# Optimization experiments

Hardware: AMD Instinct MI355X
Metric: run time of the kernel (lower is better)

Reference implementation:

```python
import jax, jax.numpy as jnp
import numpy as np

B, L = 4096, 4096

# 16 power-series exponents applied to each of the 4 physical params
PS_POWERS = jnp.array([-5.0, -4.0, -3.0, -2.0, -1.5, -1.0, -0.5, 0.0,
                       0.5, 2.0, 1.0/3.0, 3.0, 0.25, 4.0, 0.2, 5.0], dtype=jnp.float32)
# polynomial exponents of the ansatz y(eta)
POLY_POWERS = jnp.array([2.0, 5.0, 8.0, 11.0, 14.0], dtype=jnp.float32)


def setup_inputs() -> dict:
    key = jax.random.key(0)
    k1, k2, k3, k4, k5, k6 = jax.random.split(key, 6)
    # positive inputs: negative/fractional powers require x > 0
    physical_params = jax.random.uniform(k1, (B, 4), jnp.float32, minval=0.1, maxval=2.0)
    eta = jax.random.uniform(k2, (B, L), jnp.float32, minval=0.1, maxval=2.0)
    # MLP params: Linear(64, 32) and Linear(32, 5), torch layout [out, in]
    W1 = jax.random.normal(k3, (32, 64), jnp.float32) * (1.0 / np.sqrt(64.0))
    b1 = jax.random.normal(k4, (32,), jnp.float32) * 0.05
    W2 = jax.random.normal(k5, (5, 32), jnp.float32) * (1.0 / np.sqrt(32.0))
    b2 = jax.random.normal(k6, (5,), jnp.float32) * 0.05
    return {"physical_params": physical_params, "eta": eta,
            "W1": W1, "b1": b1, "W2": W2, "b2": b2}


def reference(physical_params, eta, W1, b1, W2, b2):
    # power-series transform: [B,4] -> [B,4,16] -> [B,64]
    t = (physical_params[:, :, None] ** PS_POWERS).reshape(physical_params.shape[0], -1)
    # global (scalar) normalization; torch .std() is unbiased (ddof=1)
    mean = t.mean()
    std = jnp.std(t, ddof=1)
    norm = (t - mean) / std
    # network = Sequential(ReLU, Linear(64,32), Linear(32,5)) -- ReLU first, no act between linears
    h = jnp.maximum(norm, 0.0) @ W1.T + b1            # [B, 32]
    coefficients = h @ W2.T + b2                       # [B, 5]
    # dy/deta[i,j] = sum_k c[i,k] * p_k * eta[i,j]^(p_k - 1)  (vectorizes the per-row loop)
    eta_pows = eta[:, :, None] ** (POLY_POWERS - 1.0)  # [B, L, 5]
    dy_deta = jnp.einsum('bk,bjk->bj', coefficients * POLY_POWERS, eta_pows)  # [B, L]
    return dy_deta
```

## Files before the change

### kernel.cpp

```cpp
#include <hip/hip_runtime.h>
#include <math.h>

static constexpr int B  = 4096;
static constexpr int L  = 4096;
static constexpr int NT = B * 64;
static constexpr int RED_BLOCKS  = 256;
static constexpr int RED_THREADS = 256;

__device__ __constant__ float c_ps_powers[16] = {
    -5.0f, -4.0f, -3.0f, -2.0f, -1.5f, -1.0f, -0.5f, 0.0f,
     0.5f,  2.0f,  0.33333334f, 3.0f, 0.25f, 4.0f, 0.2f, 5.0f};

__device__ __constant__ float c_poly[5] = {2.0f, 5.0f, 8.0f, 11.0f, 14.0f};

__global__ __launch_bounds__(RED_THREADS)
void k_reduce_partial(const float* __restrict__ pp, double* __restrict__ part) {
    const int tid = threadIdx.x;
    const int gid = blockIdx.x * RED_THREADS + tid;
    double s = 0.0, s2 = 0.0;
    for (int i = gid; i < NT; i += RED_BLOCKS * RED_THREADS) {
        const int b = i >> 6;
        const int j = i & 63;
        const float x = pp[(b << 2) + (j >> 4)];
        const float t = powf(x, c_ps_powers[j & 15]);
        s  += (double)t;
        s2 += (double)t * (double)t;
    }
    __shared__ double sh_s[RED_THREADS];
    __shared__ double sh_s2[RED_THREADS];
    sh_s[tid] = s; sh_s2[tid] = s2;
    __syncthreads();
    for (int off = RED_THREADS >> 1; off > 0; off >>= 1) {
        if (tid < off) {
            sh_s[tid]  += sh_s[tid + off];
            sh_s2[tid] += sh_s2[tid + off];
        }
        __syncthreads();
    }
    if (tid == 0) {
        part[blockIdx.x]              = sh_s[0];
        part[RED_BLOCKS + blockIdx.x] = sh_s2[0];
    }
}

__global__ __launch_bounds__(RED_BLOCKS)
void k_finalize(const double* __restrict__ part, float* __restrict__ stats) {
    const int tid = threadIdx.x;
    __shared__ double sh_s[RED_BLOCKS];
    __shared__ double sh_s2[RED_BLOCKS];
    sh_s[tid]  = part[tid];
    sh_s2[tid] = part[RED_BLOCKS + tid];
    __syncthreads();
    for (int off = RED_BLOCKS >> 1; off > 0; off >>= 1) {
        if (tid < off) {
            sh_s[tid]  += sh_s[tid + off];
            sh_s2[tid] += sh_s2[tid + off];
        }
        __syncthreads();
    }
    if (tid == 0) {
        const double n    = (double)NT;
        const double mean = sh_s[0] / n;
        const double var  = (sh_s2[0] - n * mean * mean) / (n - 1.0);
        stats[0] = (float)mean;
        stats[1] = (float)(1.0 / sqrt(var));
    }
}

__device__ __forceinline__ float poly_eval(float e, float c0, float c1,
                                           float c2, float c3, float c4) {
    const float e3 = e * e * e;
    float w   = e;
    float acc = c0 * w;
    w *= e3;
    acc = fmaf(c1, w, acc);
    w *= e3;
    acc = fmaf(c2, w, acc);
    w *= e3;
    acc = fmaf(c3, w, acc);
    w *= e3;
    acc = fmaf(c4, w, acc);
    return acc;
}

__global__ __launch_bounds__(256)
void k_main(const float* __restrict__ pp,  const float* __restrict__ eta,
            const float* __restrict__ W1,  const float* __restrict__ b1,
            const float* __restrict__ W2,  const float* __restrict__ b2,
            const float* __restrict__ stats, float* __restrict__ out) {
    const int row = blockIdx.x;
    const int tid = threadIdx.x;

    __shared__ float sh_r[64];
    __shared__ float sh_h[32];
    __shared__ float sh_c[5];

    const float mean    = stats[0];
    const float inv_std = stats[1];

    if (tid < 64) {
        const float x = pp[(row << 2) + (tid >> 4)];
        const float t = powf(x, c_ps_powers[tid & 15]);
        sh_r[tid] = fmaxf((t - mean) * inv_std, 0.0f);
    }
    __syncthreads();

    if (tid < 32) {
        float acc = b1[tid];
        const float* w = W1 + tid * 64;
        #pragma unroll
        for (int j = 0; j < 64; ++j) acc = fmaf(sh_r[j], w[j], acc);
        sh_h[tid] = acc;
    }
    __syncthreads();

    if (tid < 5) {
        float acc = b2[tid];
        const float* w = W2 + tid * 32;
        #pragma unroll
        for (int o = 0; o < 32; ++o) acc = fmaf(sh_h[o], w[o], acc);
        sh_c[tid] = acc * c_poly[tid];
    }
    __syncthreads();

    const float c0 = sh_c[0], c1 = sh_c[1], c2 = sh_c[2],
                c3 = sh_c[3], c4 = sh_c[4];

    const float4* ep = reinterpret_cast<const float4*>(eta + (size_t)row * L);
    float4*       op = reinterpret_cast<float4*>(out + (size_t)row * L);

    #pragma unroll
    for (int i = tid; i < L / 4; i += 256) {
        const float4 e = ep[i];
        float4 r;
        r.x = poly_eval(e.x, c0, c1, c2, c3, c4);
        r.y = poly_eval(e.y, c0, c1, c2, c3, c4);
        r.z = poly_eval(e.z, c0, c1, c2, c3, c4);
        r.w = poly_eval(e.w, c0, c1, c2, c3, c4);
        op[i] = r;
    }
}

extern "C" void kernel_launch(void* const* d_in, const int* in_sizes, int n_in,
                              void* d_out, int out_size, void* d_ws, size_t ws_size,
                              hipStream_t stream) {
    const float* pp  = (const float*)d_in[0];
    const float* eta = (const float*)d_in[1];
    const float* W1  = (const float*)d_in[2];
    const float* b1  = (const float*)d_in[3];
    const float* W2  = (const float*)d_in[4];
    const float* b2  = (const float*)d_in[5];
    float* out = (float*)d_out;

    double* part = (double*)d_ws;
    float*  stats = (float*)(part + 2 * RED_BLOCKS);

    k_reduce_partial<<<RED_BLOCKS, RED_THREADS, 0, stream>>>(pp, part);
    k_finalize<<<1, RED_BLOCKS, 0, stream>>>(part, stats);
    k_main<<<B, 256, 0, stream>>>(pp, eta, W1, b1, W2, b2, stats, out);
}
```

Before: 37.07 us.

## Merge stats reduction into one kernel, use hardware log2/exp2, nontemporal IO

Replaces the two-kernel partial/finalize reduction with one single-block kernel in which each thread loads each param once, takes log2 once and evaluates all 16 powers with hardware exp2. This removes one kernel launch and the repeated powf calls. The main kernel also uses hardware log2/exp2 for the power series and nontemporal loads/stores for the eta/out stream. Hardware approximations lower precision compared with powf, and a single block leaves most of the GPU idle during the stats phase.

```diff
diff --git a/kernel.cpp b/kernel.cpp
--- a/kernel.cpp
+++ b/kernel.cpp
@@ -3,9 +3,10 @@
 
 static constexpr int B  = 4096;
 static constexpr int L  = 4096;
-static constexpr int NT = B * 64;
-static constexpr int RED_BLOCKS  = 256;
-static constexpr int RED_THREADS = 256;
+static constexpr int NX = B * 4;
+static constexpr int STATS_THREADS = 1024;
+
+typedef float f4 __attribute__((ext_vector_type(4)));
 
 __device__ __constant__ float c_ps_powers[16] = {
     -5.0f, -4.0f, -3.0f, -2.0f, -1.5f, -1.0f, -0.5f, 0.0f,
@@ -13,24 +14,32 @@
 
 __device__ __constant__ float c_poly[5] = {2.0f, 5.0f, 8.0f, 11.0f, 14.0f};
 
-__global__ __launch_bounds__(RED_THREADS)
-void k_reduce_partial(const float* __restrict__ pp, double* __restrict__ part) {
+__device__ __forceinline__ float hw_log2(float x) { return __builtin_amdgcn_logf(x); }
+__device__ __forceinline__ float hw_exp2(float x) { return __builtin_amdgcn_exp2f(x); }
+
+__global__ __launch_bounds__(STATS_THREADS)
+void k_stats(const float* __restrict__ pp, float* __restrict__ stats) {
     const int tid = threadIdx.x;
-    const int gid = blockIdx.x * RED_THREADS + tid;
     double s = 0.0, s2 = 0.0;
-    for (int i = gid; i < NT; i += RED_BLOCKS * RED_THREADS) {
-        const int b = i >> 6;
-        const int j = i & 63;
-        const float x = pp[(b << 2) + (j >> 4)];
-        const float t = powf(x, c_ps_powers[j & 15]);
-        s  += (double)t;
-        s2 += (double)t * (double)t;
+    #pragma unroll
+    for (int k = 0; k < NX / STATS_THREADS; ++k) {
+        const float x  = pp[tid + k * STATS_THREADS];
+        const float lx = hw_log2(x);
+        float sf = 0.0f, sf2 = 0.0f;
+        #pragma unroll
+        for (int p = 0; p < 16; ++p) {
+            const float t = hw_exp2(c_ps_powers[p] * lx);
+            sf  += t;
+            sf2 = fmaf(t, t, sf2);
+        }
+        s  += (double)sf;
+        s2 += (double)sf2;
     }
-    __shared__ double sh_s[RED_THREADS];
-    __shared__ double sh_s2[RED_THREADS];
+    __shared__ double sh_s[STATS_THREADS];
+    __shared__ double sh_s2[STATS_THREADS];
     sh_s[tid] = s; sh_s2[tid] = s2;
     __syncthreads();
-    for (int off = RED_THREADS >> 1; off > 0; off >>= 1) {
+    for (int off = STATS_THREADS >> 1; off > 0; off >>= 1) {
         if (tid < off) {
             sh_s[tid]  += sh_s[tid + off];
             sh_s2[tid] += sh_s2[tid + off];
@@ -38,28 +47,7 @@
         __syncthreads();
     }
     if (tid == 0) {
-        part[blockIdx.x]              = sh_s[0];
-        part[RED_BLOCKS + blockIdx.x] = sh_s2[0];
-    }
-}
-
-__global__ __launch_bounds__(RED_BLOCKS)
-void k_finalize(const double* __restrict__ part, float* __restrict__ stats) {
-    const int tid = threadIdx.x;
-    __shared__ double sh_s[RED_BLOCKS];
-    __shared__ double sh_s2[RED_BLOCKS];
-    sh_s[tid]  = part[tid];
-    sh_s2[tid] = part[RED_BLOCKS + tid];
-    __syncthreads();
-    for (int off = RED_BLOCKS >> 1; off > 0; off >>= 1) {
-        if (tid < off) {
-            sh_s[tid]  += sh_s[tid + off];
-            sh_s2[tid] += sh_s2[tid + off];
-        }
-        __syncthreads();
-    }
-    if (tid == 0) {
-        const double n    = (double)NT;
+        const double n    = (double)(B * 64);
         const double mean = sh_s[0] / n;
         const double var  = (sh_s2[0] - n * mean * mean) / (n - 1.0);
         stats[0] = (float)mean;
@@ -95,12 +83,11 @@
     __shared__ float sh_h[32];
     __shared__ float sh_c[5];
 
-    const float mean    = stats[0];
-    const float inv_std = stats[1];
-
     if (tid < 64) {
-        const float x = pp[(row << 2) + (tid >> 4)];
-        const float t = powf(x, c_ps_powers[tid & 15]);
+        const float mean    = stats[0];
+        const float inv_std = stats[1];
+        const float x  = pp[(row << 2) + (tid >> 4)];
+        const float t  = hw_exp2(c_ps_powers[tid & 15] * hw_log2(x));
         sh_r[tid] = fmaxf((t - mean) * inv_std, 0.0f);
     }
     __syncthreads();
@@ -126,18 +113,18 @@
     const float c0 = sh_c[0], c1 = sh_c[1], c2 = sh_c[2],
                 c3 = sh_c[3], c4 = sh_c[4];
 
-    const float4* ep = reinterpret_cast<const float4*>(eta + (size_t)row * L);
-    float4*       op = reinterpret_cast<float4*>(out + (size_t)row * L);
+    const f4* ep = reinterpret_cast<const f4*>(eta + (size_t)row * L);
+    f4*       op = reinterpret_cast<f4*>(out + (size_t)row * L);
 
     #pragma unroll
     for (int i = tid; i < L / 4; i += 256) {
-        const float4 e = ep[i];
-        float4 r;
+        const f4 e = __builtin_nontemporal_load(ep + i);
+        f4 r;
         r.x = poly_eval(e.x, c0, c1, c2, c3, c4);
         r.y = poly_eval(e.y, c0, c1, c2, c3, c4);
         r.z = poly_eval(e.z, c0, c1, c2, c3, c4);
         r.w = poly_eval(e.w, c0, c1, c2, c3, c4);
-        op[i] = r;
+        __builtin_nontemporal_store(r, op + i);
     }
 }
 
@@ -152,10 +139,8 @@
     const float* b2  = (const float*)d_in[5];
     float* out = (float*)d_out;
 
-    double* part = (double*)d_ws;
-    float*  stats = (float*)(part + 2 * RED_BLOCKS);
+    float* stats = (float*)d_ws;
 
-    k_reduce_partial<<<RED_BLOCKS, RED_THREADS, 0, stream>>>(pp, part);
-    k_finalize<<<1, RED_BLOCKS, 0, stream>>>(part, stats);
+    k_stats<<<1, STATS_THREADS, 0, stream>>>(pp, stats);
     k_main<<<B, 256, 0, stream>>>(pp, eta, W1, b1, W2, b2, stats, out);
 }
```

After: 43.02 us. 1.16x slower.
